# Kernel optimization log

Measured on AMD Instinct MI355X. Metric: run time of the kernel, lower is better.

## Reference

```python
import jax, jax.numpy as jnp
import numpy as np


def gather_neighbour(pc, neighbor_idx):
    # pc: [B, N, d], neighbor_idx: [B, M, K] -> [B, M, K, d]
    return jax.vmap(lambda p, i: p[i])(pc, neighbor_idx)


def relative_pos_encoding(xyz, neigh_idx):
    # xyz: [B, N, 3], neigh_idx: [B, N, K]
    neighbor_xyz = gather_neighbour(xyz, neigh_idx)                 # [B, N, K, 3]
    xyz_tile = jnp.broadcast_to(xyz[:, :, None, :], neighbor_xyz.shape)
    relative_xyz = xyz_tile - neighbor_xyz
    relative_dis = jnp.sqrt(jnp.sum(relative_xyz * relative_xyz, axis=-1, keepdims=True))
    return jnp.concatenate([relative_dis, relative_xyz, xyz_tile, neighbor_xyz], axis=-1)  # [B,N,K,10]


def random_sample(feature, pool_idx):
    # feature: [B, d, N, 1], pool_idx: [B, Np, K] -> [B, d, Np, 1]
    feat = feature[..., 0]                                          # [B, d, N]
    B, Np, K = pool_idx.shape
    d = feat.shape[1]
    g = jnp.take_along_axis(feat, pool_idx.reshape(B, 1, Np * K), axis=2)
    g = g.reshape(B, d, Np, K)
    return jnp.max(g, axis=3, keepdims=True)


def nearest_interpolation(feature, interp_idx):
    # feature: [B, d, Np, 1], interp_idx: [B, U, 1] -> [B, d, U, 1]
    feat = feature[..., 0]                                          # [B, d, Np]
    B, U = interp_idx.shape[0], interp_idx.shape[1]
    g = jnp.take_along_axis(feat, interp_idx.reshape(B, 1, U), axis=2)
    return g[..., None]


def setup_inputs() -> dict:
    key = jax.random.key(0)
    k = jax.random.split(key, 6)
    B, N, K, d = 4, 65536, 16, 32
    Np = N // 4
    # neighbor indices that never point to self (avoids sqrt(0) NaN in bwd)
    base = jnp.arange(N, dtype=jnp.int32)[None, :, None]
    off = jax.random.randint(k[1], (B, N, K), 1, N, dtype=jnp.int32)
    neigh_idx = (base + off) % N
    return {
        "xyz": jax.random.normal(k[0], (B, N, 3), jnp.float32),
        "neigh_idx": neigh_idx,
        "feat_pool": jax.random.normal(k[2], (B, d, N, 1), jnp.float32),
        "pool_idx": jax.random.randint(k[3], (B, Np, K), 0, N, dtype=jnp.int32),
        "feat_interp": jax.random.normal(k[4], (B, d, Np, 1), jnp.float32),
        "interp_idx": jax.random.randint(k[5], (B, N, 1), 0, Np, dtype=jnp.int32),
    }


def reference(xyz, neigh_idx, feat_pool, pool_idx, feat_interp, interp_idx):
    rel = relative_pos_encoding(xyz, neigh_idx)        # [B, N, K, 10]
    pooled = random_sample(feat_pool, pool_idx)        # [B, d, Np, 1]
    interp = nearest_interpolation(feat_interp, interp_idx)  # [B, d, N, 1]
    return rel, pooled, interp
```

## Files before the change

kernel.cpp:

```cpp
#include <hip/hip_runtime.h>
#include <math.h>

#define BATCH 4
#define NPTS  65536
#define KNBR  16
#define DF    32
#define NPOOL 16384

__global__ __launch_bounds__(256) void relpos_kernel(
    const float* __restrict__ xyz, const int* __restrict__ nidx,
    float* __restrict__ out)
{
    __shared__ float s[2560];
    const int tid = threadIdx.x;
    const int e = blockIdx.x * 256 + tid;
    const int b = e >> 20;
    const int n = (e >> 4) & (NPTS - 1);
    const int j = nidx[e];
    const float* c = xyz + (size_t)(b * NPTS + n) * 3;
    const float* g = xyz + (size_t)(b * NPTS + j) * 3;
    const float cx = c[0], cy = c[1], cz = c[2];
    const float nx = g[0], ny = g[1], nz = g[2];
    const float rx = cx - nx, ry = cy - ny, rz = cz - nz;
    const float dist = sqrtf(rx * rx + ry * ry + rz * rz);
    float* st = s + tid * 10;
    st[0] = dist; st[1] = rx; st[2] = ry; st[3] = rz;
    st[4] = cx;   st[5] = cy; st[6] = cz;
    st[7] = nx;   st[8] = ny; st[9] = nz;
    __syncthreads();
    float4* o4 = (float4*)(out + (size_t)blockIdx.x * 2560);
    const float4* s4 = (const float4*)s;
    o4[tid]       = s4[tid];
    o4[tid + 256] = s4[tid + 256];
    if (tid < 128) o4[tid + 512] = s4[tid + 512];
}

__global__ __launch_bounds__(256) void transpose_kernel(
    const float* __restrict__ in, float* __restrict__ outp, int nn)
{
    __shared__ float tile[32][33];
    const int tpb = nn >> 5;
    const int b  = blockIdx.x / tpb;
    const int n0 = (blockIdx.x % tpb) << 5;
    const int t  = threadIdx.x;
    const int nl = t & 31;
    const int dl = t >> 5;
    #pragma unroll
    for (int it = 0; it < 4; ++it) {
        const int d = dl + it * 8;
        tile[d][nl] = in[(size_t)(b * DF + d) * nn + n0 + nl];
    }
    __syncthreads();
    #pragma unroll
    for (int it = 0; it < 4; ++it) {
        const int n = dl + it * 8;
        outp[((size_t)b * nn + n0 + n) * DF + nl] = tile[nl][n];
    }
}

__global__ __launch_bounds__(256) void pool_kernel_t(
    const float* __restrict__ ft, const int* __restrict__ pidx,
    float* __restrict__ out)
{
    __shared__ int   s_idx[64 * KNBR];
    __shared__ float s_out[64 * 33];
    const int t   = threadIdx.x;
    const int bpb = NPOOL / 64;
    const int b   = blockIdx.x / bpb;
    const int np0 = (blockIdx.x % bpb) * 64;
    const int4* src4 = (const int4*)(pidx + (size_t)(b * NPOOL + np0) * KNBR);
    ((int4*)s_idx)[t] = src4[t];
    __syncthreads();
    const int d = t & 31;
    const int g = t >> 5;
    const float* fb = ft + (size_t)b * NPTS * DF;
    #pragma unroll
    for (int r = 0; r < 8; ++r) {
        const int ul = g * 8 + r;
        float m = -INFINITY;
        #pragma unroll
        for (int k = 0; k < KNBR; ++k) {
            const int idx = s_idx[ul * KNBR + k];
            m = fmaxf(m, fb[(size_t)idx * DF + d]);
        }
        s_out[ul * 33 + d] = m;
    }
    __syncthreads();
    #pragma unroll
    for (int w = 0; w < 8; ++w) {
        const int flat = w * 256 + t;
        const int u  = flat & 63;
        const int dd = flat >> 6;
        out[(size_t)(b * DF + dd) * NPOOL + np0 + u] = s_out[u * 33 + dd];
    }
}

__global__ __launch_bounds__(256) void interp_kernel_t(
    const float* __restrict__ ft, const int* __restrict__ iidx,
    float* __restrict__ out)
{
    __shared__ int   s_idx[64];
    __shared__ float s_out[64 * 33];
    const int t   = threadIdx.x;
    const int bpb = NPTS / 64;
    const int b   = blockIdx.x / bpb;
    const int u0  = (blockIdx.x % bpb) * 64;
    if (t < 64) s_idx[t] = iidx[b * NPTS + u0 + t];
    __syncthreads();
    const int d = t & 31;
    const int g = t >> 5;
    const float* fb = ft + (size_t)b * NPOOL * DF;
    #pragma unroll
    for (int r = 0; r < 8; ++r) {
        const int ul = g * 8 + r;
        s_out[ul * 33 + d] = fb[(size_t)s_idx[ul] * DF + d];
    }
    __syncthreads();
    #pragma unroll
    for (int w = 0; w < 8; ++w) {
        const int flat = w * 256 + t;
        const int u  = flat & 63;
        const int dd = flat >> 6;
        out[(size_t)(b * DF + dd) * NPTS + u0 + u] = s_out[u * 33 + dd];
    }
}

__global__ __launch_bounds__(256) void pool_kernel_naive(
    const float* __restrict__ feat, const int* __restrict__ pidx,
    float* __restrict__ out)
{
    const int i  = blockIdx.x * 256 + threadIdx.x;
    const int np = i & (NPOOL - 1);
    const int bd = i >> 14;
    const int b  = bd >> 5;
    const int4* ip = (const int4*)(pidx + (size_t)(b * NPOOL + np) * KNBR);
    const float* f = feat + (size_t)bd * NPTS;
    float m = -INFINITY;
    #pragma unroll
    for (int q = 0; q < 4; ++q) {
        const int4 v = ip[q];
        m = fmaxf(m, f[v.x]); m = fmaxf(m, f[v.y]);
        m = fmaxf(m, f[v.z]); m = fmaxf(m, f[v.w]);
    }
    out[i] = m;
}

__global__ __launch_bounds__(256) void interp_kernel_naive(
    const float* __restrict__ feat, const int* __restrict__ iidx,
    float* __restrict__ out)
{
    const int i  = blockIdx.x * 256 + threadIdx.x;
    const int u  = i & (NPTS - 1);
    const int bd = i >> 16;
    const int b  = bd >> 5;
    out[i] = feat[(size_t)bd * NPOOL + iidx[b * NPTS + u]];
}

extern "C" void kernel_launch(void* const* d_in, const int* in_sizes, int n_in,
                              void* d_out, int out_size, void* d_ws, size_t ws_size,
                              hipStream_t stream) {
    const float* xyz         = (const float*)d_in[0];
    const int*   neigh_idx   = (const int*)d_in[1];
    const float* feat_pool   = (const float*)d_in[2];
    const int*   pool_idx    = (const int*)d_in[3];
    const float* feat_interp = (const float*)d_in[4];
    const int*   interp_idx  = (const int*)d_in[5];

    float* out    = (float*)d_out;
    float* rel    = out;
    float* pooled = rel + (size_t)BATCH * NPTS * KNBR * 10;
    float* interp = pooled + (size_t)BATCH * DF * NPOOL;

    relpos_kernel<<<(BATCH * NPTS * KNBR) / 256, 256, 0, stream>>>(xyz, neigh_idx, rel);

    const size_t need = ((size_t)BATCH * DF * NPTS + (size_t)BATCH * DF * NPOOL) * sizeof(float);
    if (ws_size >= need) {
        float* ftp = (float*)d_ws;
        float* fti = ftp + (size_t)BATCH * DF * NPTS;
        transpose_kernel<<<BATCH * (NPTS / 32), 256, 0, stream>>>(feat_pool, ftp, NPTS);
        transpose_kernel<<<BATCH * (NPOOL / 32), 256, 0, stream>>>(feat_interp, fti, NPOOL);
        pool_kernel_t<<<BATCH * (NPOOL / 64), 256, 0, stream>>>(ftp, pool_idx, pooled);
        interp_kernel_t<<<BATCH * (NPTS / 64), 256, 0, stream>>>(fti, interp_idx, interp);
    } else {
        pool_kernel_naive<<<(BATCH * DF * NPOOL) / 256, 256, 0, stream>>>(feat_pool, pool_idx, pooled);
        interp_kernel_naive<<<(BATCH * DF * NPTS) / 256, 256, 0, stream>>>(feat_interp, interp_idx, interp);
    }
}
```

Measured before the change: 332.7 us.

## Fuse transposes and gathers into two kernels with padded xyz and float4 gathers

Merges the two feature transposes and an xyz-to-float4 padding pass into one prep kernel. The relative-position, pooling and interpolation work then runs in a single fused kernel that interleaves block roles (16 relpos, 1 pool, 4 interp per group). The pool and interp gathers now load float4 rows, and relpos reads the padded xyz as single float4 loads. This cuts launches from five to two and improves gather vectorisation, at the cost of extra workspace and an extra write and read of the padded xyz.

```diff
diff --git a/kernel.cpp b/kernel.cpp
--- a/kernel.cpp
+++ b/kernel.cpp
@@ -6,6 +6,149 @@
 #define KNBR  16
 #define DF    32
 #define NPOOL 16384
+
+#define FTP_ELEMS   ((size_t)BATCH * NPTS * DF)
+#define FTI_ELEMS   ((size_t)BATCH * NPOOL * DF)
+#define XYZ4_ELEMS  ((size_t)BATCH * NPTS * 4)
+
+#define T1_BLKS (BATCH * (NPTS / 32))
+#define T2_BLKS (BATCH * (NPOOL / 32))
+#define T3_BLKS ((BATCH * NPTS) / 256)
+__global__ __launch_bounds__(256) void prep_kernel(
+    const float* __restrict__ feat_pool, const float* __restrict__ feat_interp,
+    const float* __restrict__ xyz,
+    float* __restrict__ ftp, float* __restrict__ fti, float* __restrict__ xyz4)
+{
+    __shared__ float tile[32][33];
+    const int bid = blockIdx.x;
+    const int t = threadIdx.x;
+    if (bid < T1_BLKS + T2_BLKS) {
+        const float* in; float* outp; int nn, tb;
+        if (bid < T1_BLKS) { in = feat_pool;  outp = ftp; nn = NPTS;  tb = bid; }
+        else               { in = feat_interp; outp = fti; nn = NPOOL; tb = bid - T1_BLKS; }
+        const int tpb = nn >> 5;
+        const int b  = tb / tpb;
+        const int n0 = (tb % tpb) << 5;
+        const int nl = t & 31;
+        const int dl = t >> 5;
+        #pragma unroll
+        for (int it = 0; it < 4; ++it) {
+            const int d = dl + it * 8;
+            tile[d][nl] = in[(size_t)(b * DF + d) * nn + n0 + nl];
+        }
+        __syncthreads();
+        #pragma unroll
+        for (int it = 0; it < 4; ++it) {
+            const int n = dl + it * 8;
+            outp[((size_t)b * nn + n0 + n) * DF + nl] = tile[nl][n];
+        }
+    } else {
+        const int p = (bid - T1_BLKS - T2_BLKS) * 256 + t;
+        const float x = xyz[(size_t)p * 3 + 0];
+        const float y = xyz[(size_t)p * 3 + 1];
+        const float z = xyz[(size_t)p * 3 + 2];
+        ((float4*)xyz4)[p] = make_float4(x, y, z, 0.f);
+    }
+}
+
+#define R_BLKS 16384
+#define P_BLKS 1024
+#define I_BLKS 4096
+#define MAIN_BLKS (R_BLKS + P_BLKS + I_BLKS)
+
+__global__ __launch_bounds__(256) void fused_main(
+    const float* __restrict__ xyz4, const int* __restrict__ nidx,
+    const float* __restrict__ ftp,  const int* __restrict__ pidx,
+    const float* __restrict__ fti,  const int* __restrict__ iidx,
+    float* __restrict__ rel, float* __restrict__ pooled, float* __restrict__ interp)
+{
+    __shared__ char smem[12800];
+    const int g = blockIdx.x / 21;
+    const int m = blockIdx.x % 21;
+    const int t = threadIdx.x;
+
+    if (m < 16) {
+        float* s = (float*)smem;
+        const int rblk = g * 16 + m;
+        const int e = rblk * 256 + t;
+        const int b = e >> 20;
+        const int n = (e >> 4) & (NPTS - 1);
+        const int j = nidx[e];
+        const float4 c = ((const float4*)xyz4)[b * NPTS + n];
+        const float4 q = ((const float4*)xyz4)[b * NPTS + j];
+        const float rx = c.x - q.x, ry = c.y - q.y, rz = c.z - q.z;
+        const float dist = sqrtf(rx * rx + ry * ry + rz * rz);
+        float* st = s + t * 10;
+        st[0] = dist; st[1] = rx;  st[2] = ry;  st[3] = rz;
+        st[4] = c.x;  st[5] = c.y; st[6] = c.z;
+        st[7] = q.x;  st[8] = q.y; st[9] = q.z;
+        __syncthreads();
+        float4* o4 = (float4*)(rel + (size_t)rblk * 2560);
+        const float4* s4 = (const float4*)s;
+        o4[t]       = s4[t];
+        o4[t + 256] = s4[t + 256];
+        if (t < 128) o4[t + 512] = s4[t + 512];
+    } else if (m == 16) {
+        int*   s_idx = (int*)smem;
+        float* s_out = (float*)(smem + 4096);
+        const int bpb = NPOOL / 64;
+        const int b   = g / bpb;
+        const int np0 = (g % bpb) * 64;
+        ((int4*)s_idx)[t] = ((const int4*)(pidx + (size_t)(b * NPOOL + np0) * KNBR))[t];
+        __syncthreads();
+        const float4* fb4 = (const float4*)(ftp + (size_t)b * NPTS * DF);
+        const int l8 = t & 7;
+        #pragma unroll
+        for (int it = 0; it < 2; ++it) {
+            const int u = (t >> 3) + it * 32;
+            float4 acc = make_float4(-INFINITY, -INFINITY, -INFINITY, -INFINITY);
+            #pragma unroll
+            for (int k = 0; k < KNBR; ++k) {
+                const int idx = s_idx[u * KNBR + k];
+                const float4 v = fb4[(size_t)idx * 8 + l8];
+                acc.x = fmaxf(acc.x, v.x); acc.y = fmaxf(acc.y, v.y);
+                acc.z = fmaxf(acc.z, v.z); acc.w = fmaxf(acc.w, v.w);
+            }
+            float* so = s_out + u * 33 + l8 * 4;
+            so[0] = acc.x; so[1] = acc.y; so[2] = acc.z; so[3] = acc.w;
+        }
+        __syncthreads();
+        #pragma unroll
+        for (int w = 0; w < 8; ++w) {
+            const int flat = w * 256 + t;
+            const int u  = flat & 63;
+            const int dd = flat >> 6;
+            pooled[(size_t)(b * DF + dd) * NPOOL + np0 + u] = s_out[u * 33 + dd];
+        }
+    } else {
+        int*   s_idx = (int*)smem;
+        float* s_out = (float*)(smem + 256);
+        const int i   = g * 4 + (m - 17);
+        const int bpb = NPTS / 64;
+        const int b   = i / bpb;
+        const int u0  = (i % bpb) * 64;
+        if (t < 64) s_idx[t] = iidx[b * NPTS + u0 + t];
+        __syncthreads();
+        const float4* fb4 = (const float4*)(fti + (size_t)b * NPOOL * DF);
+        const int l8 = t & 7;
+        #pragma unroll
+        for (int it = 0; it < 2; ++it) {
+            const int u = (t >> 3) + it * 32;
+            const int idx = s_idx[u];
+            const float4 v = fb4[(size_t)idx * 8 + l8];
+            float* so = s_out + u * 33 + l8 * 4;
+            so[0] = v.x; so[1] = v.y; so[2] = v.z; so[3] = v.w;
+        }
+        __syncthreads();
+        #pragma unroll
+        for (int w = 0; w < 8; ++w) {
+            const int flat = w * 256 + t;
+            const int u  = flat & 63;
+            const int dd = flat >> 6;
+            interp[(size_t)(b * DF + dd) * NPTS + u0 + u] = s_out[u * 33 + dd];
+        }
+    }
+}
 
 __global__ __launch_bounds__(256) void relpos_kernel(
     const float* __restrict__ xyz, const int* __restrict__ nidx,
@@ -35,96 +178,6 @@
     if (tid < 128) o4[tid + 512] = s4[tid + 512];
 }
 
-__global__ __launch_bounds__(256) void transpose_kernel(
-    const float* __restrict__ in, float* __restrict__ outp, int nn)
-{
-    __shared__ float tile[32][33];
-    const int tpb = nn >> 5;
-    const int b  = blockIdx.x / tpb;
-    const int n0 = (blockIdx.x % tpb) << 5;
-    const int t  = threadIdx.x;
-    const int nl = t & 31;
-    const int dl = t >> 5;
-    #pragma unroll
-    for (int it = 0; it < 4; ++it) {
-        const int d = dl + it * 8;
-        tile[d][nl] = in[(size_t)(b * DF + d) * nn + n0 + nl];
-    }
-    __syncthreads();
-    #pragma unroll
-    for (int it = 0; it < 4; ++it) {
-        const int n = dl + it * 8;
-        outp[((size_t)b * nn + n0 + n) * DF + nl] = tile[nl][n];
-    }
-}
-
-__global__ __launch_bounds__(256) void pool_kernel_t(
-    const float* __restrict__ ft, const int* __restrict__ pidx,
-    float* __restrict__ out)
-{
-    __shared__ int   s_idx[64 * KNBR];
-    __shared__ float s_out[64 * 33];
-    const int t   = threadIdx.x;
-    const int bpb = NPOOL / 64;
-    const int b   = blockIdx.x / bpb;
-    const int np0 = (blockIdx.x % bpb) * 64;
-    const int4* src4 = (const int4*)(pidx + (size_t)(b * NPOOL + np0) * KNBR);
-    ((int4*)s_idx)[t] = src4[t];
-    __syncthreads();
-    const int d = t & 31;
-    const int g = t >> 5;
-    const float* fb = ft + (size_t)b * NPTS * DF;
-    #pragma unroll
-    for (int r = 0; r < 8; ++r) {
-        const int ul = g * 8 + r;
-        float m = -INFINITY;
-        #pragma unroll
-        for (int k = 0; k < KNBR; ++k) {
-            const int idx = s_idx[ul * KNBR + k];
-            m = fmaxf(m, fb[(size_t)idx * DF + d]);
-        }
-        s_out[ul * 33 + d] = m;
-    }
-    __syncthreads();
-    #pragma unroll
-    for (int w = 0; w < 8; ++w) {
-        const int flat = w * 256 + t;
-        const int u  = flat & 63;
-        const int dd = flat >> 6;
-        out[(size_t)(b * DF + dd) * NPOOL + np0 + u] = s_out[u * 33 + dd];
-    }
-}
-
-__global__ __launch_bounds__(256) void interp_kernel_t(
-    const float* __restrict__ ft, const int* __restrict__ iidx,
-    float* __restrict__ out)
-{
-    __shared__ int   s_idx[64];
-    __shared__ float s_out[64 * 33];
-    const int t   = threadIdx.x;
-    const int bpb = NPTS / 64;
-    const int b   = blockIdx.x / bpb;
-    const int u0  = (blockIdx.x % bpb) * 64;
-    if (t < 64) s_idx[t] = iidx[b * NPTS + u0 + t];
-    __syncthreads();
-    const int d = t & 31;
-    const int g = t >> 5;
-    const float* fb = ft + (size_t)b * NPOOL * DF;
-    #pragma unroll
-    for (int r = 0; r < 8; ++r) {
-        const int ul = g * 8 + r;
-        s_out[ul * 33 + d] = fb[(size_t)s_idx[ul] * DF + d];
-    }
-    __syncthreads();
-    #pragma unroll
-    for (int w = 0; w < 8; ++w) {
-        const int flat = w * 256 + t;
-        const int u  = flat & 63;
-        const int dd = flat >> 6;
-        out[(size_t)(b * DF + dd) * NPTS + u0 + u] = s_out[u * 33 + dd];
-    }
-}
-
 __global__ __launch_bounds__(256) void pool_kernel_naive(
     const float* __restrict__ feat, const int* __restrict__ pidx,
     float* __restrict__ out)
@@ -171,17 +224,17 @@
     float* pooled = rel + (size_t)BATCH * NPTS * KNBR * 10;
     float* interp = pooled + (size_t)BATCH * DF * NPOOL;
 
-    relpos_kernel<<<(BATCH * NPTS * KNBR) / 256, 256, 0, stream>>>(xyz, neigh_idx, rel);
-
-    const size_t need = ((size_t)BATCH * DF * NPTS + (size_t)BATCH * DF * NPOOL) * sizeof(float);
+    const size_t need = (FTP_ELEMS + FTI_ELEMS + XYZ4_ELEMS) * sizeof(float);
     if (ws_size >= need) {
-        float* ftp = (float*)d_ws;
-        float* fti = ftp + (size_t)BATCH * DF * NPTS;
-        transpose_kernel<<<BATCH * (NPTS / 32), 256, 0, stream>>>(feat_pool, ftp, NPTS);
-        transpose_kernel<<<BATCH * (NPOOL / 32), 256, 0, stream>>>(feat_interp, fti, NPOOL);
-        pool_kernel_t<<<BATCH * (NPOOL / 64), 256, 0, stream>>>(ftp, pool_idx, pooled);
-        interp_kernel_t<<<BATCH * (NPTS / 64), 256, 0, stream>>>(fti, interp_idx, interp);
+        float* ftp  = (float*)d_ws;
+        float* fti  = ftp + FTP_ELEMS;
+        float* xyz4 = fti + FTI_ELEMS;
+        prep_kernel<<<T1_BLKS + T2_BLKS + T3_BLKS, 256, 0, stream>>>(
+            feat_pool, feat_interp, xyz, ftp, fti, xyz4);
+        fused_main<<<MAIN_BLKS, 256, 0, stream>>>(
+            xyz4, neigh_idx, ftp, pool_idx, fti, interp_idx, rel, pooled, interp);
     } else {
+        relpos_kernel<<<(BATCH * NPTS * KNBR) / 256, 256, 0, stream>>>(xyz, neigh_idx, rel);
         pool_kernel_naive<<<(BATCH * DF * NPOOL) / 256, 256, 0, stream>>>(feat_pool, pool_idx, pooled);
         interp_kernel_naive<<<(BATCH * DF * NPTS) / 256, 256, 0, stream>>>(feat_interp, interp_idx, interp);
     }
```

Result: faster. 321.9 us (-3.2%).
